# Kernel optimization log

Hardware: AMD Instinct MI355X
Metric: run time of the kernel (lower is better)

The kernel has to match this reference:

```python
import jax, jax.numpy as jnp
import numpy as np
import math

B, NI, NU, D, H, MAXNB, T = 1024, 50000, 20000, 256, 4, 20, 1000


def _cosine_sqrt_ab():
    t = jnp.linspace(0.0, T, T + 1) / T
    ab = jnp.cos((t + 0.008) / 1.008 * math.pi / 2) ** 2
    ab = ab / ab[0]
    ab = ab[1:]
    return jnp.sqrt(ab), jnp.sqrt(1.0 - ab)


def _ln(x, g, b, eps=1e-5):
    m = jnp.mean(x, -1, keepdims=True)
    v = jnp.var(x, -1, keepdims=True)
    return (x - m) / jnp.sqrt(v + eps) * g + b


def _mha(q, k, v, wqkv, bqkv, wo, bo):
    # torch nn.MultiheadAttention (batch_first) with packed in_proj
    d = q.shape[-1]
    dh = d // H
    wq, wk, wv = jnp.split(wqkv, 3, axis=0)
    bq, bk, bv = jnp.split(bqkv, 3, axis=0)
    def heads(x, w, bb):
        y = x @ w.T + bb
        return y.reshape(x.shape[0], x.shape[1], H, dh).transpose(0, 2, 1, 3)
    qh, kh, vh = heads(q, wq, bq), heads(k, wk, bk), heads(v, wv, bv)
    att = jax.nn.softmax(jnp.einsum('bhqd,bhkd->bhqk', qh, kh) / math.sqrt(dh), axis=-1)
    o = jnp.einsum('bhqk,bhkd->bhqd', att, vh)
    o = o.transpose(0, 2, 1, 3).reshape(q.shape[0], q.shape[1], d)
    return o @ wo.T + bo


def setup_inputs() -> dict:
    key = jax.random.key(0)
    ks = iter(jax.random.split(key, 64))
    p = lambda shape, s=0.02: jax.random.normal(next(ks), shape, jnp.float32) * s
    inp = {}
    inp['x0'] = (jax.random.uniform(next(ks), (B, NI)) < 0.05).astype(jnp.float32)
    inp['user_ids'] = jax.random.randint(next(ks), (B,), 0, NU)
    inp['t'] = jax.random.randint(next(ks), (B,), 0, T)
    inp['noise'] = jax.random.normal(next(ks), (B, D), jnp.float32)
    inp['neighbor_idx'] = jax.random.randint(next(ks), (NU, MAXNB), 0, NI)
    inp['item_emb'] = p((NI, D), 0.01)
    inp['enc_w1'] = p((2 * D, NI), 0.01); inp['enc_b1'] = jnp.zeros((2 * D,))
    inp['enc_w2'] = p((D, 2 * D)); inp['enc_b2'] = jnp.zeros((D,))
    inp['dec_w1'] = p((2 * D, D)); inp['dec_b1'] = jnp.zeros((2 * D,))
    inp['dec_w2'] = p((NI, 2 * D)); inp['dec_b2'] = jnp.zeros((NI,))
    inp['up_w'] = p((D, D)); inp['up_b'] = jnp.zeros((D,))
    inp['ip_w'] = p((D, D)); inp['ip_b'] = jnp.zeros((D,))
    inp['te_w1'] = p((32, 1)); inp['te_b1'] = jnp.zeros((32,))
    inp['te_w2'] = p((D, 32)); inp['te_b2'] = jnp.zeros((D,))
    inp['ca_wqkv'] = p((3 * D, D)); inp['ca_bqkv'] = jnp.zeros((3 * D,))
    inp['ca_wo'] = p((D, D)); inp['ca_bo'] = jnp.zeros((D,))
    inp['sa_wqkv'] = p((3 * D, D)); inp['sa_bqkv'] = jnp.zeros((3 * D,))
    inp['sa_wo'] = p((D, D)); inp['sa_bo'] = jnp.zeros((D,))
    inp['n1_g'] = jnp.ones((D,)); inp['n1_b'] = jnp.zeros((D,))
    inp['n2_g'] = jnp.ones((D,)); inp['n2_b'] = jnp.zeros((D,))
    inp['ff_w1'] = p((2 * D, D)); inp['ff_b1'] = jnp.zeros((2 * D,))
    inp['ff_w2'] = p((D, 2 * D)); inp['ff_b2'] = jnp.zeros((D,))
    return inp


def reference(x0, user_ids, t, noise, neighbor_idx, item_emb,
              enc_w1, enc_b1, enc_w2, enc_b2, dec_w1, dec_b1, dec_w2, dec_b2,
              up_w, up_b, ip_w, ip_b, te_w1, te_b1, te_w2, te_b2,
              ca_wqkv, ca_bqkv, ca_wo, ca_bo, sa_wqkv, sa_bqkv, sa_wo, sa_bo,
              n1_g, n1_b, n2_g, n2_b, ff_w1, ff_b1, ff_w2, ff_b2):
    gelu = lambda x: jax.nn.gelu(x, approximate=False)
    # encoder: (B, NI) -> (B, D)
    z0 = gelu(x0 @ enc_w1.T + enc_b1) @ enc_w2.T + enc_b2
    sqrt_ab, sqrt_1ab = _cosine_sqrt_ab()
    z_t = sqrt_ab[t][:, None] * z0 + sqrt_1ab[t][:, None] * noise
    # vectorized padded neighbor gather: (B, MAXNB, D)
    nb = item_emb[neighbor_idx[user_ids]]
    t_norm = t.astype(jnp.float32) / T
    # denoiser
    q = (z_t @ up_w.T + up_b)[:, None, :]
    kv = nb @ ip_w.T + ip_b
    te = jax.nn.silu(t_norm[:, None] @ te_w1.T + te_b1) @ te_w2.T + te_b2
    q = q + te[:, None, :]
    ca = _mha(q, kv, kv, ca_wqkv, ca_bqkv, ca_wo, ca_bo)
    h = _ln(q + ca, n1_g, n1_b)[:, 0, :]
    sa = _mha(h[:, None], h[:, None], h[:, None], sa_wqkv, sa_bqkv, sa_wo, sa_bo)[:, 0, :]
    h = _ln(h + sa, n2_g, n2_b)
    z_pred = h + (gelu(h @ ff_w1.T + ff_b1) @ ff_w2.T + ff_b2)
    diff_loss = jnp.mean((z_pred - z0) ** 2)
    logits = gelu(z0 @ dec_w1.T + dec_b1) @ dec_w2.T + dec_b2
    recon = jnp.mean(jax.nn.softplus(logits) - logits * x0)
    return diff_loss + 0.1 * recon
```

## Files before the change

kernel.cpp:

```cpp
#include <hip/hip_runtime.h>
#include <math.h>

#define NI   50000
#define Tt   1000
#define KP   50176
#define MW   1568
#define NPAD 50048

typedef __bf16 bf16x8 __attribute__((ext_vector_type(8)));
typedef float  f32x4  __attribute__((ext_vector_type(4)));

__device__ __forceinline__ unsigned short f2bf(float f) {
  unsigned u = __float_as_uint(f);
  u += 0x7FFFu + ((u >> 16) & 1u);
  return (unsigned short)(u >> 16);
}
__device__ __forceinline__ float bf2f(unsigned short u) {
  return __uint_as_float(((unsigned)u) << 16);
}
__device__ __forceinline__ unsigned pack2(float a, float b) {
  return (unsigned)f2bf(a) | ((unsigned)f2bf(b) << 16);
}
__device__ __forceinline__ f32x4 mfma16(const unsigned short* a, const unsigned short* b, f32x4 c) {
  typedef unsigned short u16x8 __attribute__((ext_vector_type(8)));
  u16x8 av = *(const u16x8*)a;
  u16x8 bv = *(const u16x8*)b;
  return __builtin_amdgcn_mfma_f32_16x16x32_bf16(
      __builtin_bit_cast(bf16x8, av), __builtin_bit_cast(bf16x8, bv), c, 0, 0, 0);
}
__device__ __forceinline__ float gelu_f(float x) {
  return 0.5f * x * (1.f + erff(x * 0.70710678118654752f));
}

#define GLD16(gsrc, ldst) __builtin_amdgcn_global_load_lds( \
    (const __attribute__((address_space(1))) unsigned int*)(const void*)(gsrc), \
    (__attribute__((address_space(3))) unsigned int*)(void*)(ldst), 16, 0, 0)

#define PIPE_FENCE() __builtin_amdgcn_sched_barrier(0)
#define RAW_BAR()    __builtin_amdgcn_s_barrier()

__global__ __launch_bounds__(256) void bm_expand(
    const float* __restrict__ x0, unsigned int* __restrict__ xmask)
{
  __shared__ unsigned int nib[256];
  int r = blockIdx.y, tid = threadIdx.x;
  int c0 = blockIdx.x * 2048;
  int k = c0 + tid * 8;
  const float* row = x0 + (size_t)r * NI;
  float4 a = make_float4(0.f, 0.f, 0.f, 0.f), b = a;
  if (k + 8 <= NI) {
    a = *(const float4*)(row + k);
    b = *(const float4*)(row + k + 4);
  }
  unsigned bits8 =
      (a.x != 0.f ? 1u : 0u)  | (a.y != 0.f ? 2u : 0u)  |
      (a.z != 0.f ? 4u : 0u)  | (a.w != 0.f ? 8u : 0u)  |
      (b.x != 0.f ? 16u : 0u) | (b.y != 0.f ? 32u : 0u) |
      (b.z != 0.f ? 64u : 0u) | (b.w != 0.f ? 128u : 0u);
  nib[tid] = bits8;
  __syncthreads();
  if (tid < 64) {
    unsigned wv = nib[tid * 4] | (nib[tid * 4 + 1] << 8) |
                  (nib[tid * 4 + 2] << 16) | (nib[tid * 4 + 3] << 24);
    int widx = (c0 >> 5) + tid;
    if (widx < MW) xmask[(size_t)r * MW + widx] = wv;
  }
}

__global__ __launch_bounds__(256) void cvt_w1(const float* __restrict__ src,
                                              unsigned short* __restrict__ dst) {
  int c = blockIdx.x * 2048 + threadIdx.x * 8;
  if (c >= KP) return;
  int r = blockIdx.y;
  const float* s = src + (size_t)r * NI;
  uint4 o;
  if (c + 8 <= NI) {
    float4 a = *(const float4*)(s + c), b = *(const float4*)(s + c + 4);
    o.x = pack2(a.x, a.y); o.y = pack2(a.z, a.w);
    o.z = pack2(b.x, b.y); o.w = pack2(b.z, b.w);
  } else {
    float v[8];
#pragma unroll
    for (int i = 0; i < 8; ++i) v[i] = (c + i < NI) ? s[c + i] : 0.f;
    o.x = pack2(v[0], v[1]); o.y = pack2(v[2], v[3]);
    o.z = pack2(v[4], v[5]); o.w = pack2(v[6], v[7]);
  }
  *(uint4*)(dst + (size_t)r * KP + c) = o;
}

__global__ __launch_bounds__(256) void cvt_w2n(const float* __restrict__ src,
                                               unsigned short* __restrict__ dst) {
  size_t idx = ((size_t)blockIdx.x * 256 + threadIdx.x) * 8;
  float4 a = *(const float4*)(src + idx), b = *(const float4*)(src + idx + 4);
  uint4 o;
  o.x = pack2(a.x, a.y); o.y = pack2(a.z, a.w);
  o.z = pack2(b.x, b.y); o.w = pack2(b.z, b.w);
  *(uint4*)(dst + idx) = o;
}

__global__ __launch_bounds__(256) void cvt_many(
    const float* s0, const float* s1, const float* s2, const float* s3,
    const float* s4, const float* s5, const float* s6,
    unsigned short* d0, unsigned short* d1, unsigned short* d2, unsigned short* d3,
    unsigned short* d4, unsigned short* d5, unsigned short* d6)
{
  const float* srcs[7] = {s0, s1, s2, s3, s4, s5, s6};
  unsigned short* dsts[7] = {d0, d1, d2, d3, d4, d5, d6};
  const int ns[7] = {131072, 65536, 65536, 65536, 131072, 131072, 131072};
  int j = blockIdx.y;
  int i = (blockIdx.x * 256 + threadIdx.x) * 8;
  if (i >= ns[j]) return;
  float4 a = *(const float4*)(srcs[j] + i), b = *(const float4*)(srcs[j] + i + 4);
  uint4 o;
  o.x = pack2(a.x, a.y); o.y = pack2(a.z, a.w);
  o.z = pack2(b.x, b.y); o.w = pack2(b.z, b.w);
  *(uint4*)(dsts[j] + i) = o;
}

__global__ __launch_bounds__(256) void compose_k(
    const float* __restrict__ ca_wqkv, const float* __restrict__ ca_bqkv,
    const float* __restrict__ ip_w, const float* __restrict__ ip_b,
    const float* __restrict__ sa_wqkv, const float* __restrict__ sa_bqkv,
    const float* __restrict__ sa_wo, const float* __restrict__ sa_bo,
    unsigned short* __restrict__ Wkv, float* __restrict__ bkv,
    unsigned short* __restrict__ Wsa, float* __restrict__ bsa)
{
  int b = blockIdx.x, k = threadIdx.x;
  if (b < 512) {
    const float* wrow = ca_wqkv + (size_t)(256 + b) * 256;
    float s = 0.f;
    for (int c = 0; c < 256; ++c) s += wrow[c] * ip_w[c * 256 + k];
    Wkv[b * 256 + k] = f2bf(s);
    if (k == 0) {
      float sb = 0.f;
      for (int c = 0; c < 256; ++c) sb += wrow[c] * ip_b[c];
      bkv[b] = sb + ca_bqkv[256 + b];
    }
  } else {
    int i = b - 512;
    const float* worow = sa_wo + (size_t)i * 256;
    float s = 0.f;
    for (int c = 0; c < 256; ++c) s += worow[c] * sa_wqkv[(512 + c) * 256 + k];
    Wsa[i * 256 + k] = f2bf(s);
    if (k == 0) {
      float sb = 0.f;
      for (int c = 0; c < 256; ++c) sb += worow[c] * sa_bqkv[512 + c];
      bsa[i] = sb + sa_bo[i];
    }
  }
}

__global__ __launch_bounds__(256) void enc_gemm(
    const unsigned int* __restrict__ xmask,
    const unsigned short* __restrict__ Bw,
    float* __restrict__ P0, float* __restrict__ P1)
{
  __shared__ __align__(16) unsigned short As[128 * 32];
  __shared__ __align__(16) unsigned short Bs[2][128 * 32];
  const int tid = threadIdx.x;
  const int id = blockIdx.x;
  const int g = (id & 7) + 8 * (id >> 6);
  const int m0 = ((id >> 3) & 7) * 128;
  const int n0 = (g & 3) * 128;
  const int kc = g >> 2;
  const int kb = kc * 1568;
  const int w = tid >> 6, l = tid & 63;
  const int wm = (w >> 1) * 64, wn = (w & 1) * 64;
  const int fr = l & 15, fo = (l >> 4) * 8;
  const int s0 = tid, s1 = tid + 256;
  const unsigned short* Br0 = Bw + (size_t)(n0 + (s0 >> 2)) * KP + kb + (s0 & 3) * 8;
  const unsigned short* Br1 = Bw + (size_t)(n0 + (s1 >> 2)) * KP + kb + (s1 & 3) * 8;
  const int arow = tid >> 1, ahalf = tid & 1;
  const unsigned int* mrowp = xmask + (size_t)(m0 + arow) * MW + (kb >> 5);
  f32x4 acc[4][4] = {};

#define EXPANDA(VW) do {                                                     \
    unsigned bits_ = ((VW) >> (ahalf * 16)) & 0xFFFFu;                       \
    uint4 q0_, q1_;                                                          \
    q0_.x = (bits_ & 1u     ? 0x3F80u : 0u) | (bits_ & 2u     ? 0x3F800000u : 0u); \
    q0_.y = (bits_ & 4u     ? 0x3F80u : 0u) | (bits_ & 8u     ? 0x3F800000u : 0u); \
    q0_.z = (bits_ & 16u    ? 0x3F80u : 0u) | (bits_ & 32u    ? 0x3F800000u : 0u); \
    q0_.w = (bits_ & 64u    ? 0x3F80u : 0u) | (bits_ & 128u   ? 0x3F800000u : 0u); \
    q1_.x = (bits_ & 256u   ? 0x3F80u : 0u) | (bits_ & 512u   ? 0x3F800000u : 0u); \
    q1_.y = (bits_ & 1024u  ? 0x3F80u : 0u) | (bits_ & 2048u  ? 0x3F800000u : 0u); \
    q1_.z = (bits_ & 4096u  ? 0x3F80u : 0u) | (bits_ & 8192u  ? 0x3F800000u : 0u); \
    q1_.w = (bits_ & 16384u ? 0x3F80u : 0u) | (bits_ & 32768u ? 0x3F800000u : 0u); \
    *(uint4*)&As[arow * 32 + ahalf * 16]     = q0_;                          \
    *(uint4*)&As[arow * 32 + ahalf * 16 + 8] = q1_;                          \
  } while (0)

#define CMPE(BUF) do {                                                       \
    const unsigned short *ap_[4], *bp_[4];                                   \
    _Pragma("unroll") for (int i_ = 0; i_ < 4; ++i_) {                       \
      ap_[i_] = &As[(wm + 16 * i_ + fr) * 32 + fo];                          \
      bp_[i_] = &Bs[BUF][(wn + 16 * i_ + fr) * 32 + fo]; }                   \
    _Pragma("unroll") for (int i_ = 0; i_ < 4; ++i_)                         \
    _Pragma("unroll") for (int j_ = 0; j_ < 4; ++j_)                         \
      acc[i_][j_] = mfma16(ap_[i_], bp_[j_], acc[i_][j_]); } while (0)

  {
    unsigned vm = mrowp[0];
    GLD16(Br0,      &Bs[0][s0 * 8]);
    GLD16(Br1,      &Bs[0][s1 * 8]);
    GLD16(Br0 + 32, &Bs[1][s0 * 8]);
    GLD16(Br1 + 32, &Bs[1][s1 * 8]);
    EXPANDA(vm);
    asm volatile("s_waitcnt vmcnt(2) lgkmcnt(0)" ::: "memory");
    PIPE_FENCE(); RAW_BAR(); PIPE_FENCE();
  }
  for (int it = 0; it < 49; ++it) {
    unsigned vnext = 0;
    if (it < 48) vnext = mrowp[it + 1];
    CMPE(it & 1);
    if (it == 48) break;
    PIPE_FENCE(); RAW_BAR(); PIPE_FENCE();
    if (it < 47) {
      GLD16(Br0 + (it + 2) * 32, &Bs[it & 1][s0 * 8]);
      GLD16(Br1 + (it + 2) * 32, &Bs[it & 1][s1 * 8]);
    }
    EXPANDA(vnext);
    if (it < 47) asm volatile("s_waitcnt vmcnt(2) lgkmcnt(0)" ::: "memory");
    else         asm volatile("s_waitcnt vmcnt(0) lgkmcnt(0)" ::: "memory");
    PIPE_FENCE(); RAW_BAR(); PIPE_FENCE();
  }
#undef EXPANDA
#undef CMPE

  const int cr = (l >> 4) * 4, cc = l & 15;
  float* Cp = ((kc < 16) ? P0 : P1) + (size_t)(kc & 15) * 524288;
#pragma unroll
  for (int i = 0; i < 4; ++i)
#pragma unroll
    for (int j = 0; j < 4; ++j) {
      int n = n0 + wn + 16 * j + cc;
#pragma unroll
      for (int r = 0; r < 4; ++r) {
        int m = m0 + wm + 16 * i + cr + r;
        Cp[(size_t)m * 512 + n] = acc[i][j][r];
      }
    }
}

template<int T>
__global__ __launch_bounds__(256) void gemm128(
    const unsigned short* __restrict__ A, int lda,
    const unsigned short* __restrict__ Bw, int ldb,
    const float* __restrict__ bias, void* __restrict__ Cv, int ldc, int K,
    const unsigned int* __restrict__ xmask, float* __restrict__ loss, int Nvalid)
{
  __shared__ __align__(16) unsigned short As[128 * 32];
  __shared__ __align__(16) unsigned short Bs[128 * 32];
  __shared__ unsigned int msk[128][4];
  __shared__ float red[4];
  const int tid = threadIdx.x;
  int m0, n0, iters;
  if (T == 1) {
    int id = blockIdx.x;
    int n = (id & 7) + 8 * (id >> 6);
    if (n >= 391) return;
    m0 = ((id >> 3) & 7) * 128;
    n0 = n * 128;
    iters = 16;
  } else {
    m0 = blockIdx.x * 128; n0 = blockIdx.y * 128;
    iters = K >> 5;
  }
  const int w = tid >> 6, l = tid & 63;
  const int wm = (w >> 1) * 64, wn = (w & 1) * 64;
  const int fr = l & 15, fo = (l >> 4) * 8;
  const int s0 = tid, s1 = tid + 256;
  f32x4 acc[4][4] = {};
  for (int it = 0; it < iters; ++it) {
    int k0 = it * 32;
    __syncthreads();
    GLD16(A  + (size_t)(m0 + (s0 >> 2)) * lda + k0 + (s0 & 3) * 8, &As[s0 * 8]);
    GLD16(A  + (size_t)(m0 + (s1 >> 2)) * lda + k0 + (s1 & 3) * 8, &As[s1 * 8]);
    GLD16(Bw + (size_t)(n0 + (s0 >> 2)) * ldb + k0 + (s0 & 3) * 8, &Bs[s0 * 8]);
    GLD16(Bw + (size_t)(n0 + (s1 >> 2)) * ldb + k0 + (s1 & 3) * 8, &Bs[s1 * 8]);
    __syncthreads();
    const unsigned short *ap[4], *bp[4];
#pragma unroll
    for (int i = 0; i < 4; ++i) {
      ap[i] = &As[(wm + 16 * i + fr) * 32 + fo];
      bp[i] = &Bs[(wn + 16 * i + fr) * 32 + fo];
    }
#pragma unroll
    for (int i = 0; i < 4; ++i)
#pragma unroll
      for (int j = 0; j < 4; ++j)
        acc[i][j] = mfma16(ap[i], bp[j], acc[i][j]);
  }
  const int cr = (l >> 4) * 4, cc = l & 15;
  if (T == 0) {
    unsigned short* Cb = (unsigned short*)Cv;
#pragma unroll
    for (int j = 0; j < 4; ++j) {
      int n = n0 + wn + 16 * j + cc;
      float bv = bias[n];
#pragma unroll
      for (int i = 0; i < 4; ++i)
#pragma unroll
        for (int r = 0; r < 4; ++r) {
          int m = m0 + wm + 16 * i + cr + r;
          Cb[(size_t)m * ldc + n] = f2bf(acc[i][j][r] + bv);
        }
    }
  } else {
    {
      int row = tid >> 1, p = tid & 1;
      *(uint2*)&msk[row][p * 2] =
          *(const uint2*)(xmask + (size_t)(m0 + row) * MW + (n0 >> 5) + p * 2);
    }
    __syncthreads();
    float ts = 0.f;
#pragma unroll
    for (int j = 0; j < 4; ++j) {
      int nl = wn + 16 * j + cc;
      int n = n0 + nl;
      if (n < Nvalid) {
        float bv = bias[n];
#pragma unroll
        for (int i = 0; i < 4; ++i)
#pragma unroll
          for (int r = 0; r < 4; ++r) {
            int ml = wm + 16 * i + cr + r;
            float lg = acc[i][j][r] + bv;
            float sp = fmaxf(lg, 0.f) + __logf(1.f + __expf(-fabsf(lg)));
            unsigned word = msk[ml][nl >> 5];
            ts += sp - (((word >> (nl & 31)) & 1u) ? lg : 0.f);
          }
      }
    }
    for (int off = 32; off > 0; off >>= 1) ts += __shfl_xor(ts, off);
    if (l == 0) red[w] = ts;
    __syncthreads();
    if (tid == 0) atomicAdd(loss, red[0] + red[1] + red[2] + red[3]);
  }
}

template<int EPI>
__global__ __launch_bounds__(256) void gemm64(
    const unsigned short* __restrict__ A, int lda,
    const unsigned short* __restrict__ Bw, int ldb,
    const float* __restrict__ bias, void* __restrict__ Cv, int ldc, int K,
    const void* __restrict__ R0, const void* __restrict__ R1, const void* __restrict__ R2,
    void* __restrict__ W0, void* __restrict__ W1, float* __restrict__ loss)
{
  __shared__ __align__(16) unsigned short As[64 * 32];
  __shared__ __align__(16) unsigned short Bs[64 * 32];
  __shared__ float red[4];
  const int tid = threadIdx.x;
  const int m0 = blockIdx.x * 64, n0 = blockIdx.y * 64;
  const int w = tid >> 6, l = tid & 63;
  const int wm = (w >> 1) * 32, wn = (w & 1) * 32;
  const int fr = l & 15, fo = (l >> 4) * 8;
  const int srow = tid >> 2, scol = (tid & 3) * 8;
  f32x4 acc[2][2] = {};
  for (int k0 = 0; k0 < K; k0 += 32) {
    __syncthreads();
    GLD16(A  + (size_t)(m0 + srow) * lda + k0 + scol, &As[tid * 8]);
    GLD16(Bw + (size_t)(n0 + srow) * ldb + k0 + scol, &Bs[tid * 8]);
    __syncthreads();
    const unsigned short* ap0 = &As[(wm +      fr) * 32 + fo];
    const unsigned short* ap1 = &As[(wm + 16 + fr) * 32 + fo];
    const unsigned short* bp0 = &Bs[(wn +      fr) * 32 + fo];
    const unsigned short* bp1 = &Bs[(wn + 16 + fr) * 32 + fo];
    acc[0][0] = mfma16(ap0, bp0, acc[0][0]);
    acc[0][1] = mfma16(ap0, bp1, acc[0][1]);
    acc[1][0] = mfma16(ap1, bp0, acc[1][0]);
    acc[1][1] = mfma16(ap1, bp1, acc[1][1]);
  }
  const int cr = (l >> 4) * 4, cc = l & 15;
  float ts = 0.f;
#pragma unroll
  for (int i = 0; i < 2; ++i)
#pragma unroll
    for (int j = 0; j < 2; ++j) {
      int n = n0 + wn + 16 * j + cc;
      float bv = bias[n];
#pragma unroll
      for (int r = 0; r < 4; ++r) {
        int m = m0 + wm + 16 * i + cr + r;
        float v = acc[i][j][r] + bv;
        size_t idx = (size_t)m * ldc + n;
        if (EPI == 0) ((float*)Cv)[idx] = v;
        if (EPI == 1) ((unsigned short*)Cv)[idx] = f2bf(v);
        if (EPI == 2) ((unsigned short*)Cv)[idx] = f2bf(gelu_f(v));
        if (EPI == 3) {
          ((float*)Cv)[idx] = v;
          ((unsigned short*)W0)[idx] = f2bf(v);
          float zt = ((const float*)R1)[m] * v +
                     ((const float*)R2)[m] * ((const float*)R0)[idx];
          ((unsigned short*)W1)[idx] = f2bf(zt);
        }
        if (EPI == 4) {
          v += ((const float*)R0)[idx];
          ((unsigned short*)Cv)[idx] = f2bf(v);
        }
        if (EPI == 5) {
          v += bf2f(((const unsigned short*)R0)[idx]);
          float d = v - ((const float*)R1)[idx];
          ts += d * d;
        }
      }
    }
  if (EPI == 5) {
    for (int off = 32; off > 0; off >>= 1) ts += __shfl_xor(ts, off);
    if (l == 0) red[w] = ts;
    __syncthreads();
    if (tid == 0) atomicAdd(loss, red[0] + red[1] + red[2] + red[3]);
  }
}

__global__ __launch_bounds__(256) void h1_epi(const float* __restrict__ P0,
                                              const float* __restrict__ P1,
                                              const float* __restrict__ b,
                                              unsigned short* __restrict__ H) {
  int i = blockIdx.x * 256 + threadIdx.x;
  float s = b[i & 511];
#pragma unroll
  for (int k = 0; k < 16; ++k) s += P0[(size_t)k * 524288 + i];
#pragma unroll
  for (int k = 0; k < 16; ++k) s += P1[(size_t)k * 524288 + i];
  H[i] = f2bf(gelu_f(s));
}

__global__ __launch_bounds__(256) void prep_te(
    const int* __restrict__ t,
    const float* __restrict__ te_w1, const float* __restrict__ te_b1,
    const float* __restrict__ te_w2, const float* __restrict__ te_b2,
    float* __restrict__ te, float* __restrict__ sab, float* __restrict__ s1ab)
{
  __shared__ float sj[32];
  int b = blockIdx.x, d = threadIdx.x;
  int ti = t[b];
  float tn = (float)ti / (float)Tt;
  if (d < 32) {
    float a = tn * te_w1[d] + te_b1[d];
    sj[d] = a / (1.f + __expf(-a));
  }
  if (d == 0) {
    double tt = (double)(ti + 1) / (double)Tt;
    double c  = cos((tt + 0.008) / 1.008 * M_PI * 0.5);
    double c0 = cos((0.008) / 1.008 * M_PI * 0.5);
    double ab = (c * c) / (c0 * c0);
    sab[b]  = (float)sqrt(ab);
    s1ab[b] = (float)sqrt(1.0 - ab);
  }
  __syncthreads();
  float accv = te_b2[d];
#pragma unroll
  for (int j = 0; j < 32; ++j) accv += sj[j] * te_w2[d * 32 + j];
  te[(size_t)b * 256 + d] = accv;
}

__global__ __launch_bounds__(256) void gather_nb(
    const int* __restrict__ uid, const int* __restrict__ nidx,
    const float* __restrict__ emb, unsigned short* __restrict__ nb)
{
  int b = blockIdx.x, j = blockIdx.y, d = threadIdx.x;
  int idx = nidx[uid[b] * 20 + j];
  nb[((size_t)b * 20 + j) * 256 + d] = f2bf(emb[(size_t)idx * 256 + d]);
}

__global__ __launch_bounds__(256) void attn_k(
    const float* __restrict__ qh, const unsigned short* __restrict__ kvh,
    unsigned short* __restrict__ o)
{
  int b = blockIdx.x, tid = threadIdx.x;
  int h = tid >> 6, d = tid & 63;
  float qv = qh[(size_t)b * 256 + h * 64 + d];
  const unsigned short* kbase = kvh + (size_t)b * 20 * 512 + h * 64 + d;
  const unsigned short* vbase = kbase + 256;
  float s[20];
#pragma unroll
  for (int k = 0; k < 20; ++k) {
    float p = qv * bf2f(kbase[k * 512]);
    for (int off = 32; off > 0; off >>= 1) p += __shfl_xor(p, off);
    s[k] = p * 0.125f;
  }
  float mx = s[0];
#pragma unroll
  for (int k = 1; k < 20; ++k) mx = fmaxf(mx, s[k]);
  float sum = 0.f;
#pragma unroll
  for (int k = 0; k < 20; ++k) { s[k] = __expf(s[k] - mx); sum += s[k]; }
  float inv = 1.f / sum;
  float ov = 0.f;
#pragma unroll
  for (int k = 0; k < 20; ++k) ov += s[k] * bf2f(vbase[k * 512]);
  o[(size_t)b * 256 + h * 64 + d] = f2bf(ov * inv);
}

__global__ __launch_bounds__(256) void ln_k(
    const unsigned short* __restrict__ X, const unsigned short* __restrict__ Y,
    const float* __restrict__ g, const float* __restrict__ bb,
    unsigned short* __restrict__ out)
{
  __shared__ float rs[4], rs2[4];
  int b = blockIdx.x, d = threadIdx.x;
  size_t i = (size_t)b * 256 + d;
  float v = bf2f(X[i]) + bf2f(Y[i]);
  float s = v, s2 = v * v;
  for (int off = 32; off > 0; off >>= 1) { s += __shfl_xor(s, off); s2 += __shfl_xor(s2, off); }
  int w = d >> 6, l = d & 63;
  if (l == 0) { rs[w] = s; rs2[w] = s2; }
  __syncthreads();
  s  = rs[0] + rs[1] + rs[2] + rs[3];
  s2 = rs2[0] + rs2[1] + rs2[2] + rs2[3];
  float mean = s * (1.f / 256.f);
  float var  = s2 * (1.f / 256.f) - mean * mean;
  out[i] = f2bf((v - mean) * rsqrtf(var + 1e-5f) * g[d] + bb[d]);
}

__global__ void final_k(const float* __restrict__ scal, float* __restrict__ out) {
  out[0] = scal[0] * (1.f / (1024.f * 256.f)) + 0.1f * scal[1] * (1.f / (1024.f * 50000.f));
}

extern "C" void kernel_launch(void* const* d_in, const int* in_sizes, int n_in,
                              void* d_out, int out_size, void* d_ws, size_t ws_size,
                              hipStream_t stream) {
  const float* x0      = (const float*)d_in[0];
  const int*   uid     = (const int*)  d_in[1];
  const int*   t       = (const int*)  d_in[2];
  const float* noise   = (const float*)d_in[3];
  const int*   nidx    = (const int*)  d_in[4];
  const float* item_emb= (const float*)d_in[5];
  const float* enc_w1  = (const float*)d_in[6];
  const float* enc_b1  = (const float*)d_in[7];
  const float* enc_w2  = (const float*)d_in[8];
  const float* enc_b2  = (const float*)d_in[9];
  const float* dec_w1  = (const float*)d_in[10];
  const float* dec_b1  = (const float*)d_in[11];
  const float* dec_w2  = (const float*)d_in[12];
  const float* dec_b2  = (const float*)d_in[13];
  const float* up_w    = (const float*)d_in[14];
  const float* up_b    = (const float*)d_in[15];
  const float* ip_w    = (const float*)d_in[16];
  const float* ip_b    = (const float*)d_in[17];
  const float* te_w1   = (const float*)d_in[18];
  const float* te_b1   = (const float*)d_in[19];
  const float* te_w2   = (const float*)d_in[20];
  const float* te_b2   = (const float*)d_in[21];
  const float* ca_wqkv = (const float*)d_in[22];
  const float* ca_bqkv = (const float*)d_in[23];
  const float* ca_wo   = (const float*)d_in[24];
  const float* ca_bo   = (const float*)d_in[25];
  const float* sa_wqkv = (const float*)d_in[26];
  const float* sa_bqkv = (const float*)d_in[27];
  const float* sa_wo   = (const float*)d_in[28];
  const float* sa_bo   = (const float*)d_in[29];
  const float* n1_g    = (const float*)d_in[30];
  const float* n1_b    = (const float*)d_in[31];
  const float* n2_g    = (const float*)d_in[32];
  const float* n2_b    = (const float*)d_in[33];
  const float* ff_w1   = (const float*)d_in[34];
  const float* ff_b1   = (const float*)d_in[35];
  const float* ff_w2   = (const float*)d_in[36];
  const float* ff_b2   = (const float*)d_in[37];
  (void)in_sizes; (void)n_in; (void)out_size; (void)ws_size;

  float* ws   = (float*)d_ws;
  float* scal = ws;
  float* sab  = ws + 4;
  float* s1ab = sab + 1024;
  float* te   = s1ab + 1024;
  float* qhf  = te + 262144;
  float* z0f  = qhf + 262144;
  float* bkv  = z0f + 262144;
  float* bsa  = bkv + 512;
  unsigned int* xmask = (unsigned int*)(bsa + 256);
  unsigned short* sh  = (unsigned short*)(xmask + 1024 * MW);
  float*          OUTp = (float*)sh;
  unsigned short* nbb  = sh;
  unsigned short* kvhb = nbb + 5242880;
  unsigned short* f1b  = kvhb + 10485760;
  unsigned short* Gb   = f1b + 524288;
  unsigned short* x0b  = Gb + 524288;
  unsigned short* w2n  = x0b;
  unsigned short* w1b  = x0b + (size_t)1024 * KP;
  unsigned short* H1b  = w1b + (size_t)512 * KP;
  unsigned short* z0b  = H1b + 524288;
  unsigned short* ztb  = z0b + 262144;
  unsigned short* qpb  = ztb + 262144;
  unsigned short* ob   = qpb + 262144;
  unsigned short* cab  = ob  + 262144;
  unsigned short* hb   = cab + 262144;
  unsigned short* saob = hb  + 262144;
  unsigned short* h2b  = saob+ 262144;
  unsigned short* enc_w2b = h2b + 262144;
  unsigned short* up_wb   = enc_w2b + 131072;
  unsigned short* ca_wqb  = up_wb + 65536;
  unsigned short* ca_wob  = ca_wqb + 65536;
  unsigned short* ff_w1b  = ca_wob + 65536;
  unsigned short* ff_w2b  = ff_w1b + 131072;
  unsigned short* dec_w1b = ff_w2b + 131072;
  unsigned short* Wkv     = dec_w1b + 131072;
  unsigned short* Wsab    = Wkv + 131072;
  float*          OUTp2   = (float*)(Wsab + 131072);

  hipMemsetAsync(scal, 0, 4 * sizeof(float), stream);

  prep_te<<<1024, 256, 0, stream>>>(t, te_w1, te_b1, te_w2, te_b2, te, sab, s1ab);
  bm_expand<<<dim3(25, 1024), 256, 0, stream>>>(x0, xmask);
  cvt_w1<<<dim3(25, 512), 256, 0, stream>>>(enc_w1, w1b);
  cvt_many<<<dim3(64, 7), 256, 0, stream>>>(enc_w2, up_w, ca_wqkv, ca_wo, ff_w1, ff_w2, dec_w1,
                                            enc_w2b, up_wb, ca_wqb, ca_wob, ff_w1b, ff_w2b, dec_w1b);
  compose_k<<<768, 256, 0, stream>>>(ca_wqkv, ca_bqkv, ip_w, ip_b,
                                     sa_wqkv, sa_bqkv, sa_wo, sa_bo,
                                     Wkv, bkv, Wsab, bsa);

  enc_gemm<<<1024, 256, 0, stream>>>(xmask, w1b, OUTp, OUTp2);
  h1_epi<<<2048, 256, 0, stream>>>(OUTp, OUTp2, enc_b1, H1b);

  cvt_w2n<<<12500, 256, 0, stream>>>(dec_w2, w2n);

  gather_nb<<<dim3(1024, 20), 256, 0, stream>>>(uid, nidx, item_emb, nbb);
  gemm128<0><<<dim3(160, 4), 256, 0, stream>>>(
      nbb, 256, Wkv, 256, bkv, kvhb, 512, 256, nullptr, nullptr, 0);

  gemm64<3><<<dim3(16, 4), 256, 0, stream>>>(
      H1b, 512, enc_w2b, 512, enc_b2, z0f, 256, 512, noise, sab, s1ab, z0b, ztb, nullptr);

  gemm64<4><<<dim3(16, 4), 256, 0, stream>>>(
      ztb, 256, up_wb, 256, up_b, qpb, 256, 256, te, nullptr, nullptr, nullptr, nullptr, nullptr);
  gemm64<0><<<dim3(16, 4), 256, 0, stream>>>(
      qpb, 256, ca_wqb, 256, ca_bqkv, qhf, 256, 256,
      nullptr, nullptr, nullptr, nullptr, nullptr, nullptr);

  attn_k<<<1024, 256, 0, stream>>>(qhf, kvhb, ob);
  gemm64<1><<<dim3(16, 4), 256, 0, stream>>>(
      ob, 256, ca_wob, 256, ca_bo, cab, 256, 256,
      nullptr, nullptr, nullptr, nullptr, nullptr, nullptr);
  ln_k<<<1024, 256, 0, stream>>>(qpb, cab, n1_g, n1_b, hb);

  gemm64<1><<<dim3(16, 4), 256, 0, stream>>>(
      hb, 256, Wsab, 256, bsa, saob, 256, 256,
      nullptr, nullptr, nullptr, nullptr, nullptr, nullptr);
  ln_k<<<1024, 256, 0, stream>>>(hb, saob, n2_g, n2_b, h2b);

  gemm64<2><<<dim3(16, 8), 256, 0, stream>>>(
      h2b, 256, ff_w1b, 256, ff_b1, f1b, 512, 256,
      nullptr, nullptr, nullptr, nullptr, nullptr, nullptr);
  gemm64<5><<<dim3(16, 4), 256, 0, stream>>>(
      f1b, 512, ff_w2b, 512, ff_b2, nullptr, 256, 512,
      h2b, z0f, nullptr, nullptr, nullptr, &scal[0]);

  gemm64<2><<<dim3(16, 8), 256, 0, stream>>>(
      z0b, 256, dec_w1b, 256, dec_b1, Gb, 512, 256,
      nullptr, nullptr, nullptr, nullptr, nullptr, nullptr);
  gemm128<1><<<3136, 256, 0, stream>>>(
      Gb, 512, w2n, 512, dec_b2, nullptr, 0, 512, xmask, &scal[1], NI);

  final_k<<<1, 1, 0, stream>>>(scal, (float*)d_out);
}
```

Measured before the change: 877.7 us.

## Merge prep kernels into one launch and expand encoder mask via LDS lookup table

Six preprocessing kernels (te prep, bitmask expand, enc_w1/dec_w2/misc bf16 conversions, weight composition) are folded into a single block-dispatched mega_prep kernel, removing launch overhead and letting independent work fill the device together. In enc_gemm, the per-iteration bitmask expansion into an A tile is replaced by async-loading mask words into LDS and indexing a 256-entry bf16 lookup table directly as MFMA A operands. This drops the A-tile stores and the extra barrier work from the loop, at the cost of extra LDS reads through the lookup indirection, which may cause bank conflicts.

```diff
diff --git a/kernel.cpp b/kernel.cpp
--- a/kernel.cpp
+++ b/kernel.cpp
@@ -35,118 +35,150 @@
 #define GLD16(gsrc, ldst) __builtin_amdgcn_global_load_lds( \
     (const __attribute__((address_space(1))) unsigned int*)(const void*)(gsrc), \
     (__attribute__((address_space(3))) unsigned int*)(void*)(ldst), 16, 0, 0)
+#define GLD4(gsrc, ldst) __builtin_amdgcn_global_load_lds( \
+    (const __attribute__((address_space(1))) unsigned int*)(const void*)(gsrc), \
+    (__attribute__((address_space(3))) unsigned int*)(void*)(ldst), 4, 0, 0)
 
 #define PIPE_FENCE() __builtin_amdgcn_sched_barrier(0)
 #define RAW_BAR()    __builtin_amdgcn_s_barrier()
 
-__global__ __launch_bounds__(256) void bm_expand(
-    const float* __restrict__ x0, unsigned int* __restrict__ xmask)
-{
-  __shared__ unsigned int nib[256];
-  int r = blockIdx.y, tid = threadIdx.x;
-  int c0 = blockIdx.x * 2048;
-  int k = c0 + tid * 8;
-  const float* row = x0 + (size_t)r * NI;
-  float4 a = make_float4(0.f, 0.f, 0.f, 0.f), b = a;
-  if (k + 8 <= NI) {
-    a = *(const float4*)(row + k);
-    b = *(const float4*)(row + k + 4);
-  }
-  unsigned bits8 =
-      (a.x != 0.f ? 1u : 0u)  | (a.y != 0.f ? 2u : 0u)  |
-      (a.z != 0.f ? 4u : 0u)  | (a.w != 0.f ? 8u : 0u)  |
-      (b.x != 0.f ? 16u : 0u) | (b.y != 0.f ? 32u : 0u) |
-      (b.z != 0.f ? 64u : 0u) | (b.w != 0.f ? 128u : 0u);
-  nib[tid] = bits8;
-  __syncthreads();
-  if (tid < 64) {
-    unsigned wv = nib[tid * 4] | (nib[tid * 4 + 1] << 8) |
-                  (nib[tid * 4 + 2] << 16) | (nib[tid * 4 + 3] << 24);
-    int widx = (c0 >> 5) + tid;
-    if (widx < MW) xmask[(size_t)r * MW + widx] = wv;
-  }
-}
-
-__global__ __launch_bounds__(256) void cvt_w1(const float* __restrict__ src,
-                                              unsigned short* __restrict__ dst) {
-  int c = blockIdx.x * 2048 + threadIdx.x * 8;
-  if (c >= KP) return;
-  int r = blockIdx.y;
-  const float* s = src + (size_t)r * NI;
-  uint4 o;
-  if (c + 8 <= NI) {
-    float4 a = *(const float4*)(s + c), b = *(const float4*)(s + c + 4);
-    o.x = pack2(a.x, a.y); o.y = pack2(a.z, a.w);
-    o.z = pack2(b.x, b.y); o.w = pack2(b.z, b.w);
-  } else {
-    float v[8];
-#pragma unroll
-    for (int i = 0; i < 8; ++i) v[i] = (c + i < NI) ? s[c + i] : 0.f;
-    o.x = pack2(v[0], v[1]); o.y = pack2(v[2], v[3]);
-    o.z = pack2(v[4], v[5]); o.w = pack2(v[6], v[7]);
-  }
-  *(uint4*)(dst + (size_t)r * KP + c) = o;
-}
-
-__global__ __launch_bounds__(256) void cvt_w2n(const float* __restrict__ src,
-                                               unsigned short* __restrict__ dst) {
-  size_t idx = ((size_t)blockIdx.x * 256 + threadIdx.x) * 8;
-  float4 a = *(const float4*)(src + idx), b = *(const float4*)(src + idx + 4);
-  uint4 o;
-  o.x = pack2(a.x, a.y); o.y = pack2(a.z, a.w);
-  o.z = pack2(b.x, b.y); o.w = pack2(b.z, b.w);
-  *(uint4*)(dst + idx) = o;
-}
-
-__global__ __launch_bounds__(256) void cvt_many(
+#define MB_BM   25600
+#define MB_W1   38400
+#define MB_W2N  50900
+#define MB_MANY 51348
+#define MB_COMP 52116
+#define MB_TE   53140
+
+__global__ __launch_bounds__(256) void mega_prep(
+    const float* __restrict__ x0, unsigned int* __restrict__ xmask,
+    const float* __restrict__ enc_w1, unsigned short* __restrict__ w1b,
+    const float* __restrict__ dec_w2, unsigned short* __restrict__ w2n,
     const float* s0, const float* s1, const float* s2, const float* s3,
     const float* s4, const float* s5, const float* s6,
     unsigned short* d0, unsigned short* d1, unsigned short* d2, unsigned short* d3,
-    unsigned short* d4, unsigned short* d5, unsigned short* d6)
-{
-  const float* srcs[7] = {s0, s1, s2, s3, s4, s5, s6};
-  unsigned short* dsts[7] = {d0, d1, d2, d3, d4, d5, d6};
-  const int ns[7] = {131072, 65536, 65536, 65536, 131072, 131072, 131072};
-  int j = blockIdx.y;
-  int i = (blockIdx.x * 256 + threadIdx.x) * 8;
-  if (i >= ns[j]) return;
-  float4 a = *(const float4*)(srcs[j] + i), b = *(const float4*)(srcs[j] + i + 4);
-  uint4 o;
-  o.x = pack2(a.x, a.y); o.y = pack2(a.z, a.w);
-  o.z = pack2(b.x, b.y); o.w = pack2(b.z, b.w);
-  *(uint4*)(dsts[j] + i) = o;
-}
-
-__global__ __launch_bounds__(256) void compose_k(
+    unsigned short* d4, unsigned short* d5, unsigned short* d6,
     const float* __restrict__ ca_wqkv, const float* __restrict__ ca_bqkv,
     const float* __restrict__ ip_w, const float* __restrict__ ip_b,
     const float* __restrict__ sa_wqkv, const float* __restrict__ sa_bqkv,
     const float* __restrict__ sa_wo, const float* __restrict__ sa_bo,
     unsigned short* __restrict__ Wkv, float* __restrict__ bkv,
-    unsigned short* __restrict__ Wsa, float* __restrict__ bsa)
+    unsigned short* __restrict__ Wsa, float* __restrict__ bsa,
+    const int* __restrict__ t,
+    const float* __restrict__ te_w1, const float* __restrict__ te_b1,
+    const float* __restrict__ te_w2, const float* __restrict__ te_b2,
+    float* __restrict__ te, float* __restrict__ sab, float* __restrict__ s1ab)
 {
-  int b = blockIdx.x, k = threadIdx.x;
-  if (b < 512) {
-    const float* wrow = ca_wqkv + (size_t)(256 + b) * 256;
-    float s = 0.f;
-    for (int c = 0; c < 256; ++c) s += wrow[c] * ip_w[c * 256 + k];
-    Wkv[b * 256 + k] = f2bf(s);
-    if (k == 0) {
-      float sb = 0.f;
-      for (int c = 0; c < 256; ++c) sb += wrow[c] * ip_b[c];
-      bkv[b] = sb + ca_bqkv[256 + b];
+  __shared__ unsigned int nib[256];
+  __shared__ float sj[32];
+  const int id = blockIdx.x, tid = threadIdx.x;
+
+  if (id < MB_BM) {
+    int r = id / 25, chunk = id % 25;
+    int c0 = chunk * 2048;
+    int k = c0 + tid * 8;
+    const float* row = x0 + (size_t)r * NI;
+    float4 a = make_float4(0.f, 0.f, 0.f, 0.f), b = a;
+    if (k + 8 <= NI) {
+      a = *(const float4*)(row + k);
+      b = *(const float4*)(row + k + 4);
+    }
+    unsigned bits8 =
+        (a.x != 0.f ? 1u : 0u)  | (a.y != 0.f ? 2u : 0u)  |
+        (a.z != 0.f ? 4u : 0u)  | (a.w != 0.f ? 8u : 0u)  |
+        (b.x != 0.f ? 16u : 0u) | (b.y != 0.f ? 32u : 0u) |
+        (b.z != 0.f ? 64u : 0u) | (b.w != 0.f ? 128u : 0u);
+    nib[tid] = bits8;
+    __syncthreads();
+    if (tid < 64) {
+      unsigned wv = nib[tid * 4] | (nib[tid * 4 + 1] << 8) |
+                    (nib[tid * 4 + 2] << 16) | (nib[tid * 4 + 3] << 24);
+      int widx = (c0 >> 5) + tid;
+      if (widx < MW) xmask[(size_t)r * MW + widx] = wv;
+    }
+  } else if (id < MB_W1) {
+    int q = id - MB_BM;
+    int r = q / 25, chunk = q % 25;
+    int c = chunk * 2048 + tid * 8;
+    if (c >= KP) return;
+    const float* s = enc_w1 + (size_t)r * NI;
+    uint4 o;
+    if (c + 8 <= NI) {
+      float4 a = *(const float4*)(s + c), b = *(const float4*)(s + c + 4);
+      o.x = pack2(a.x, a.y); o.y = pack2(a.z, a.w);
+      o.z = pack2(b.x, b.y); o.w = pack2(b.z, b.w);
+    } else {
+      float v[8];
+#pragma unroll
+      for (int i = 0; i < 8; ++i) v[i] = (c + i < NI) ? s[c + i] : 0.f;
+      o.x = pack2(v[0], v[1]); o.y = pack2(v[2], v[3]);
+      o.z = pack2(v[4], v[5]); o.w = pack2(v[6], v[7]);
+    }
+    *(uint4*)(w1b + (size_t)r * KP + c) = o;
+  } else if (id < MB_W2N) {
+    size_t idx = ((size_t)(id - MB_W1) * 256 + tid) * 8;
+    float4 a = *(const float4*)(dec_w2 + idx), b = *(const float4*)(dec_w2 + idx + 4);
+    uint4 o;
+    o.x = pack2(a.x, a.y); o.y = pack2(a.z, a.w);
+    o.z = pack2(b.x, b.y); o.w = pack2(b.z, b.w);
+    *(uint4*)(w2n + idx) = o;
+  } else if (id < MB_MANY) {
+    const float* srcs[7] = {s0, s1, s2, s3, s4, s5, s6};
+    unsigned short* dsts[7] = {d0, d1, d2, d3, d4, d5, d6};
+    const int ns[7] = {131072, 65536, 65536, 65536, 131072, 131072, 131072};
+    int q = id - MB_W2N;
+    int j = q >> 6;
+    int i = ((q & 63) * 256 + tid) * 8;
+    if (i >= ns[j]) return;
+    float4 a = *(const float4*)(srcs[j] + i), b = *(const float4*)(srcs[j] + i + 4);
+    uint4 o;
+    o.x = pack2(a.x, a.y); o.y = pack2(a.z, a.w);
+    o.z = pack2(b.x, b.y); o.w = pack2(b.z, b.w);
+    *(uint4*)(dsts[j] + i) = o;
+  } else if (id < MB_COMP) {
+    int b = id - MB_MANY, k = tid;
+    if (b < 512) {
+      const float* wrow = ca_wqkv + (size_t)(256 + b) * 256;
+      float s = 0.f;
+      for (int c = 0; c < 256; ++c) s += wrow[c] * ip_w[c * 256 + k];
+      Wkv[b * 256 + k] = f2bf(s);
+      if (k == 0) {
+        float sb = 0.f;
+        for (int c = 0; c < 256; ++c) sb += wrow[c] * ip_b[c];
+        bkv[b] = sb + ca_bqkv[256 + b];
+      }
+    } else {
+      int i = b - 512;
+      const float* worow = sa_wo + (size_t)i * 256;
+      float s = 0.f;
+      for (int c = 0; c < 256; ++c) s += worow[c] * sa_wqkv[(512 + c) * 256 + k];
+      Wsa[i * 256 + k] = f2bf(s);
+      if (k == 0) {
+        float sb = 0.f;
+        for (int c = 0; c < 256; ++c) sb += worow[c] * sa_bqkv[512 + c];
+        bsa[i] = sb + sa_bo[i];
+      }
     }
   } else {
-    int i = b - 512;
-    const float* worow = sa_wo + (size_t)i * 256;
-    float s = 0.f;
-    for (int c = 0; c < 256; ++c) s += worow[c] * sa_wqkv[(512 + c) * 256 + k];
-    Wsa[i * 256 + k] = f2bf(s);
-    if (k == 0) {
-      float sb = 0.f;
-      for (int c = 0; c < 256; ++c) sb += worow[c] * sa_bqkv[512 + c];
-      bsa[i] = sb + sa_bo[i];
-    }
+    int b = id - MB_COMP, d = tid;
+    int ti = t[b];
+    float tn = (float)ti / (float)Tt;
+    if (d < 32) {
+      float a = tn * te_w1[d] + te_b1[d];
+      sj[d] = a / (1.f + __expf(-a));
+    }
+    if (d == 0) {
+      double tt = (double)(ti + 1) / (double)Tt;
+      double c  = cos((tt + 0.008) / 1.008 * M_PI * 0.5);
+      double c0 = cos((0.008) / 1.008 * M_PI * 0.5);
+      double ab = (c * c) / (c0 * c0);
+      sab[b]  = (float)sqrt(ab);
+      s1ab[b] = (float)sqrt(1.0 - ab);
+    }
+    __syncthreads();
+    float accv = te_b2[d];
+#pragma unroll
+    for (int j = 0; j < 32; ++j) accv += sj[j] * te_w2[d * 32 + j];
+    te[(size_t)b * 256 + d] = accv;
   }
 }
 
@@ -155,8 +187,9 @@
     const unsigned short* __restrict__ Bw,
     float* __restrict__ P0, float* __restrict__ P1)
 {
-  __shared__ __align__(16) unsigned short As[128 * 32];
   __shared__ __align__(16) unsigned short Bs[2][128 * 32];
+  __shared__ __align__(16) unsigned short lut[256][8];
+  __shared__ unsigned int mskb[2][4][64];
   const int tid = threadIdx.x;
   const int id = blockIdx.x;
   const int g = (id & 7) + 8 * (id >> 6);
@@ -170,60 +203,58 @@
   const int s0 = tid, s1 = tid + 256;
   const unsigned short* Br0 = Bw + (size_t)(n0 + (s0 >> 2)) * KP + kb + (s0 & 3) * 8;
   const unsigned short* Br1 = Bw + (size_t)(n0 + (s1 >> 2)) * KP + kb + (s1 & 3) * 8;
-  const int arow = tid >> 1, ahalf = tid & 1;
-  const unsigned int* mrowp = xmask + (size_t)(m0 + arow) * MW + (kb >> 5);
+  const unsigned int* msrc = xmask + (size_t)(m0 + wm + l) * MW + (kb >> 5);
   f32x4 acc[4][4] = {};
 
-#define EXPANDA(VW) do {                                                     \
-    unsigned bits_ = ((VW) >> (ahalf * 16)) & 0xFFFFu;                       \
-    uint4 q0_, q1_;                                                          \
-    q0_.x = (bits_ & 1u     ? 0x3F80u : 0u) | (bits_ & 2u     ? 0x3F800000u : 0u); \
-    q0_.y = (bits_ & 4u     ? 0x3F80u : 0u) | (bits_ & 8u     ? 0x3F800000u : 0u); \
-    q0_.z = (bits_ & 16u    ? 0x3F80u : 0u) | (bits_ & 32u    ? 0x3F800000u : 0u); \
-    q0_.w = (bits_ & 64u    ? 0x3F80u : 0u) | (bits_ & 128u   ? 0x3F800000u : 0u); \
-    q1_.x = (bits_ & 256u   ? 0x3F80u : 0u) | (bits_ & 512u   ? 0x3F800000u : 0u); \
-    q1_.y = (bits_ & 1024u  ? 0x3F80u : 0u) | (bits_ & 2048u  ? 0x3F800000u : 0u); \
-    q1_.z = (bits_ & 4096u  ? 0x3F80u : 0u) | (bits_ & 8192u  ? 0x3F800000u : 0u); \
-    q1_.w = (bits_ & 16384u ? 0x3F80u : 0u) | (bits_ & 32768u ? 0x3F800000u : 0u); \
-    *(uint4*)&As[arow * 32 + ahalf * 16]     = q0_;                          \
-    *(uint4*)&As[arow * 32 + ahalf * 16 + 8] = q1_;                          \
-  } while (0)
+  {
+    unsigned b = (unsigned)tid;
+    uint4 q;
+    q.x = (b & 1u   ? 0x3F80u : 0u) | (b & 2u   ? 0x3F800000u : 0u);
+    q.y = (b & 4u   ? 0x3F80u : 0u) | (b & 8u   ? 0x3F800000u : 0u);
+    q.z = (b & 16u  ? 0x3F80u : 0u) | (b & 32u  ? 0x3F800000u : 0u);
+    q.w = (b & 64u  ? 0x3F80u : 0u) | (b & 128u ? 0x3F800000u : 0u);
+    *(uint4*)&lut[tid][0] = q;
+  }
+
+#define STGE(IT, BUF) do {                                   \
+    GLD4(msrc + (IT), &mskb[BUF][w][0]);                     \
+    GLD16(Br0 + (IT) * 32, &Bs[BUF][s0 * 8]);                \
+    GLD16(Br1 + (IT) * 32, &Bs[BUF][s1 * 8]); } while (0)
 
 #define CMPE(BUF) do {                                                       \
-    const unsigned short *ap_[4], *bp_[4];                                   \
-    _Pragma("unroll") for (int i_ = 0; i_ < 4; ++i_) {                       \
-      ap_[i_] = &As[(wm + 16 * i_ + fr) * 32 + fo];                          \
-      bp_[i_] = &Bs[BUF][(wn + 16 * i_ + fr) * 32 + fo]; }                   \
+    unsigned w0_ = mskb[BUF][w][fr];                                         \
+    unsigned w1_ = mskb[BUF][w][16 + fr];                                    \
+    unsigned w2_ = mskb[BUF][w][32 + fr];                                    \
+    unsigned w3_ = mskb[BUF][w][48 + fr];                                    \
+    const unsigned short* ap_[4];                                            \
+    ap_[0] = &lut[(w0_ >> fo) & 0xFF][0];                                    \
+    ap_[1] = &lut[(w1_ >> fo) & 0xFF][0];                                    \
+    ap_[2] = &lut[(w2_ >> fo) & 0xFF][0];                                    \
+    ap_[3] = &lut[(w3_ >> fo) & 0xFF][0];                                    \
+    const unsigned short* bp_[4];                                            \
+    _Pragma("unroll") for (int j_ = 0; j_ < 4; ++j_)                         \
+      bp_[j_] = &Bs[BUF][(wn + 16 * j_ + fr) * 32 + fo];                     \
     _Pragma("unroll") for (int i_ = 0; i_ < 4; ++i_)                         \
     _Pragma("unroll") for (int j_ = 0; j_ < 4; ++j_)                         \
       acc[i_][j_] = mfma16(ap_[i_], bp_[j_], acc[i_][j_]); } while (0)
 
-  {
-    unsigned vm = mrowp[0];
-    GLD16(Br0,      &Bs[0][s0 * 8]);
-    GLD16(Br1,      &Bs[0][s1 * 8]);
-    GLD16(Br0 + 32, &Bs[1][s0 * 8]);
-    GLD16(Br1 + 32, &Bs[1][s1 * 8]);
-    EXPANDA(vm);
-    asm volatile("s_waitcnt vmcnt(2) lgkmcnt(0)" ::: "memory");
-    PIPE_FENCE(); RAW_BAR(); PIPE_FENCE();
-  }
+  STGE(0, 0);
+  STGE(1, 1);
+  asm volatile("s_waitcnt vmcnt(3) lgkmcnt(0)" ::: "memory");
+  PIPE_FENCE(); RAW_BAR(); PIPE_FENCE();
   for (int it = 0; it < 49; ++it) {
-    unsigned vnext = 0;
-    if (it < 48) vnext = mrowp[it + 1];
     CMPE(it & 1);
     if (it == 48) break;
     PIPE_FENCE(); RAW_BAR(); PIPE_FENCE();
     if (it < 47) {
-      GLD16(Br0 + (it + 2) * 32, &Bs[it & 1][s0 * 8]);
-      GLD16(Br1 + (it + 2) * 32, &Bs[it & 1][s1 * 8]);
-    }
-    EXPANDA(vnext);
-    if (it < 47) asm volatile("s_waitcnt vmcnt(2) lgkmcnt(0)" ::: "memory");
-    else         asm volatile("s_waitcnt vmcnt(0) lgkmcnt(0)" ::: "memory");
+      STGE(it + 2, it & 1);
+      asm volatile("s_waitcnt vmcnt(3) lgkmcnt(0)" ::: "memory");
+    } else {
+      asm volatile("s_waitcnt vmcnt(0) lgkmcnt(0)" ::: "memory");
+    }
     PIPE_FENCE(); RAW_BAR(); PIPE_FENCE();
   }
-#undef EXPANDA
+#undef STGE
 #undef CMPE
 
   const int cr = (l >> 4) * 4, cc = l & 15;
@@ -423,35 +454,6 @@
 #pragma unroll
   for (int k = 0; k < 16; ++k) s += P1[(size_t)k * 524288 + i];
   H[i] = f2bf(gelu_f(s));
-}
-
-__global__ __launch_bounds__(256) void prep_te(
-    const int* __restrict__ t,
-    const float* __restrict__ te_w1, const float* __restrict__ te_b1,
-    const float* __restrict__ te_w2, const float* __restrict__ te_b2,
-    float* __restrict__ te, float* __restrict__ sab, float* __restrict__ s1ab)
-{
-  __shared__ float sj[32];
-  int b = blockIdx.x, d = threadIdx.x;
-  int ti = t[b];
-  float tn = (float)ti / (float)Tt;
-  if (d < 32) {
-    float a = tn * te_w1[d] + te_b1[d];
-    sj[d] = a / (1.f + __expf(-a));
-  }
-  if (d == 0) {
-    double tt = (double)(ti + 1) / (double)Tt;
-    double c  = cos((tt + 0.008) / 1.008 * M_PI * 0.5);
-    double c0 = cos((0.008) / 1.008 * M_PI * 0.5);
-    double ab = (c * c) / (c0 * c0);
-    sab[b]  = (float)sqrt(ab);
-    s1ab[b] = (float)sqrt(1.0 - ab);
-  }
-  __syncthreads();
-  float accv = te_b2[d];
-#pragma unroll
-  for (int j = 0; j < 32; ++j) accv += sj[j] * te_w2[d * 32 + j];
-  te[(size_t)b * 256 + d] = accv;
 }
 
 __global__ __launch_bounds__(256) void gather_nb(
@@ -601,19 +603,16 @@
 
   hipMemsetAsync(scal, 0, 4 * sizeof(float), stream);
 
-  prep_te<<<1024, 256, 0, stream>>>(t, te_w1, te_b1, te_w2, te_b2, te, sab, s1ab);
-  bm_expand<<<dim3(25, 1024), 256, 0, stream>>>(x0, xmask);
-  cvt_w1<<<dim3(25, 512), 256, 0, stream>>>(enc_w1, w1b);
-  cvt_many<<<dim3(64, 7), 256, 0, stream>>>(enc_w2, up_w, ca_wqkv, ca_wo, ff_w1, ff_w2, dec_w1,
-                                            enc_w2b, up_wb, ca_wqb, ca_wob, ff_w1b, ff_w2b, dec_w1b);
-  compose_k<<<768, 256, 0, stream>>>(ca_wqkv, ca_bqkv, ip_w, ip_b,
-                                     sa_wqkv, sa_bqkv, sa_wo, sa_bo,
-                                     Wkv, bkv, Wsab, bsa);
+  mega_prep<<<MB_TE, 256, 0, stream>>>(
+      x0, xmask, enc_w1, w1b, dec_w2, w2n,
+      enc_w2, up_w, ca_wqkv, ca_wo, ff_w1, ff_w2, dec_w1,
+      enc_w2b, up_wb, ca_wqb, ca_wob, ff_w1b, ff_w2b, dec_w1b,
+      ca_wqkv, ca_bqkv, ip_w, ip_b, sa_wqkv, sa_bqkv, sa_wo, sa_bo,
+      Wkv, bkv, Wsab, bsa,
+      t, te_w1, te_b1, te_w2, te_b2, te, sab, s1ab);
 
   enc_gemm<<<1024, 256, 0, stream>>>(xmask, w1b, OUTp, OUTp2);
   h1_epi<<<2048, 256, 0, stream>>>(OUTp, OUTp2, enc_b1, H1b);
-
-  cvt_w2n<<<12500, 256, 0, stream>>>(dec_w2, w2n);
 
   gather_nb<<<dim3(1024, 20), 256, 0, stream>>>(uid, nidx, item_emb, nbb);
   gemm128<0><<<dim3(160, 4), 256, 0, stream>>>(
```

Measured after the change: 855.6 us. 2.5% less time.
